# Optimization experiments

Hardware: AMD Instinct MI355X
Metric: run time of the kernel (lower is better)

Reference implementation:

```python
import jax, jax.numpy as jnp
import numpy as np

B, M, T, D, V = 16, 4096, 4, 256, 40000
HOPS, NLAYER, CONV_MAX = 3, 3, 512
PAD = 1  # PAD_token: embedding row zeroed (padding_idx)


def setup_inputs() -> dict:
    key = jax.random.key(0)
    ks = jax.random.split(key, 10)
    story = jax.random.randint(ks[0], (B, M, T), 0, V)
    conv_len = jax.random.randint(ks[1], (B,), 1, CONV_MAX)
    kb_len = jax.random.randint(ks[2], (B,), 0, M - CONV_MAX)
    query = jax.random.normal(ks[3], (B, 1, D), jnp.float32)
    history_outputs = jax.random.normal(ks[4], (B, CONV_MAX, D), jnp.float32)
    query_vector = jax.random.normal(ks[5], (B, D), jnp.float32)
    global_pointer = jax.random.uniform(ks[6], (B, M), jnp.float32)
    # hop+1 embedding tables, N(0, 0.1), padding row zeroed
    C_emb = jax.random.normal(ks[7], (HOPS + 1, V, D), jnp.float32) * 0.1
    C_emb = C_emb.at[:, PAD, :].set(0.0)
    Tg_w = jax.random.normal(ks[8], (HOPS + 1, D, D), jnp.float32) * 0.05
    Tg_b = jnp.zeros((HOPS + 1, D), jnp.float32)
    FW_w = jax.random.normal(ks[9], (D, D), jnp.float32) * 0.05
    FW_b = jnp.zeros((D,), jnp.float32)
    return dict(story=story, kb_len=kb_len, conv_len=conv_len, query=query,
                history_outputs=history_outputs, query_vector=query_vector,
                global_pointer=global_pointer, C_emb=C_emb, Tg_w=Tg_w,
                Tg_b=Tg_b, FW_w=FW_w, FW_b=FW_b)


def _add_lm(mem, kb_len, conv_len, hist):
    # mem: [B,M,D]; add hist[b, 0:conv_len[b]] into mem[b, kb_len[b]:kb_len[b]+conv_len[b]]
    j = jnp.arange(mem.shape[1])[None, :]                       # [1,M]
    start = kb_len[:, None]
    mask = (j >= start) & (j < start + conv_len[:, None])       # [B,M]
    idx = jnp.clip(j - start, 0, hist.shape[1] - 1)             # [B,M]
    gathered = jnp.take_along_axis(hist, idx[..., None], axis=1)  # [B,M,D]
    return mem + jnp.where(mask[..., None], gathered, 0.0)


def _embed(table, story, kb_len, conv_len, hist):
    # bag-of-words over the mem-token axis, then LM-embedding add
    e = jnp.sum(table[story], axis=2)                           # [B,M,D]
    return _add_lm(e, kb_len, conv_len, hist)


def reference(story, kb_len, conv_len, query, history_outputs, query_vector,
              global_pointer, C_emb, Tg_w, Tg_b, FW_w, FW_b):
    # ---- load_memory (eval mode: dropout is identity; ablationH/G = False) ----
    q = query[:, 0, :]                                          # [B,D]
    last_u = None
    m_story = None
    for layer in range(NLAYER):
        iq = q
        if layer > 0:
            g = jax.nn.sigmoid(iq @ Tg_w[0].T + Tg_b[0])
            iq = last_u[0] * g + iq * (1.0 - g)
        u = [iq]
        m_story = []
        embC = None
        for hop in range(HOPS):
            embA = _embed(C_emb[hop], story, kb_len, conv_len, history_outputs)
            logit = jnp.einsum('bmd,bd->bm', embA, u[-1])
            prob = jax.nn.softmax(logit, axis=1)
            embC = _embed(C_emb[hop + 1], story, kb_len, conv_len, history_outputs)
            o_k = jnp.einsum('bm,bmd->bd', prob, embC)
            u_k = u[-1] + o_k
            if layer > 0:
                g = jax.nn.sigmoid(u_k @ Tg_w[hop + 1].T + Tg_b[hop + 1])
                u_k = last_u[hop + 1] * g + u_k * (1.0 - g)
            u.append(u_k)
            m_story.append(embA)
        m_story.append(embC)
        last_u = u
        q = jax.nn.relu(u[-1] @ FW_w.T + FW_b)
    # ---- forward (decoder-side read over last layer's memories) ----
    uf = query_vector
    psoft = None
    logits = None
    for hop in range(HOPS):
        mA = m_story[hop] * global_pointer[:, :, None]
        logits = jnp.einsum('bmd,bd->bm', mA, uf)
        psoft = jax.nn.softmax(logits, axis=1)
        mC = m_story[hop + 1] * global_pointer[:, :, None]
        uf = uf + jnp.einsum('bm,bmd->bd', psoft, mC)
    return (psoft, logits, uf, m_story[-1])
```

## Files before the change

kernel.cpp:

```cpp
#include <hip/hip_runtime.h>
#include <math.h>

#define Bdim 16
#define Mdim 4096
#define Tdim 4
#define Ddim 256
#define Vdim 40000
#define CONVMAX 512
#define MT 64

__global__ void init_kernel(const float* __restrict__ qv, float* __restrict__ uf) {
    int b = blockIdx.x, i = threadIdx.x;
    uf[(size_t)b * Ddim + i] = qv[(size_t)b * Ddim + i];
}

__global__ void qk_kernel(const int* __restrict__ story, const int* __restrict__ kb_len,
                          const int* __restrict__ conv_len, const float* __restrict__ hist,
                          const float* __restrict__ tab, const float* __restrict__ uf,
                          const float* __restrict__ gp, float* __restrict__ logits) {
    int tid = threadIdx.x, wave = tid >> 6, lane = tid & 63;
    int row0 = blockIdx.x * 16 + wave * 4;
    int b = row0 >> 12;
    int d4 = lane * 4;
    const float4 uv = *(const float4*)(uf + (size_t)b * Ddim + d4);
    int kb = kb_len[b], cl = conv_len[b];
#pragma unroll
    for (int r = 0; r < 4; ++r) {
        int row = row0 + r;
        int m = row & (Mdim - 1);
        const int* st = story + (size_t)row * Tdim;
        float4 acc = make_float4(0.f, 0.f, 0.f, 0.f);
#pragma unroll
        for (int t = 0; t < Tdim; ++t) {
            const float4 v = *(const float4*)(tab + (size_t)st[t] * Ddim + d4);
            acc.x += v.x; acc.y += v.y; acc.z += v.z; acc.w += v.w;
        }
        if (m >= kb && m < kb + cl) {
            const float4 h = *(const float4*)(hist + ((size_t)b * CONVMAX + (m - kb)) * Ddim + d4);
            acc.x += h.x; acc.y += h.y; acc.z += h.z; acc.w += h.w;
        }
        float p = acc.x * uv.x + acc.y * uv.y + acc.z * uv.z + acc.w * uv.w;
#pragma unroll
        for (int off = 32; off > 0; off >>= 1) p += __shfl_xor(p, off, 64);
        if (lane == 0) logits[row] = p * gp[row];
    }
}

__global__ void stats_kernel(const float* __restrict__ logits, float* __restrict__ maxv,
                             float* __restrict__ rsum) {
    int b = blockIdx.x, tid = threadIdx.x;
    __shared__ float sh[256];
    const float* lg = logits + (size_t)b * Mdim;
    float mx = -INFINITY;
    for (int i = tid; i < Mdim; i += 256) mx = fmaxf(mx, lg[i]);
    sh[tid] = mx; __syncthreads();
    for (int s = 128; s > 0; s >>= 1) { if (tid < s) sh[tid] = fmaxf(sh[tid], sh[tid + s]); __syncthreads(); }
    float bm = sh[0]; __syncthreads();
    float sm = 0.f;
    for (int i = tid; i < Mdim; i += 256) sm += expf(lg[i] - bm);
    sh[tid] = sm; __syncthreads();
    for (int s = 128; s > 0; s >>= 1) { if (tid < s) sh[tid] += sh[tid + s]; __syncthreads(); }
    if (tid == 0) { maxv[b] = bm; rsum[b] = 1.0f / sh[0]; }
}

__global__ void att_kernel(const int* __restrict__ story, const int* __restrict__ kb_len,
                           const int* __restrict__ conv_len, const float* __restrict__ hist,
                           const float* __restrict__ tab, const float* __restrict__ logits,
                           const float* __restrict__ maxv, const float* __restrict__ rsum,
                           const float* __restrict__ gp,
                           float* __restrict__ uf_acc, float* __restrict__ out_m,
                           float* __restrict__ out_psoft) {
    int bid = blockIdx.x;
    int b  = bid / (Mdim / MT);
    int m0 = (bid % (Mdim / MT)) * MT;
    int tid = threadIdx.x, wave = tid >> 6, lane = tid & 63;
    int d4 = lane * 4;
    __shared__ float prob[MT];
    __shared__ float4 red[4][64];
    if (tid < MT) {
        size_t row = (size_t)b * Mdim + m0 + tid;
        float pn = expf(logits[row] - maxv[b]) * rsum[b];
        if (out_psoft) out_psoft[row] = pn;
        prob[tid] = pn * gp[row];
    }
    __syncthreads();
    int kb = kb_len[b], cl = conv_len[b];
    float4 acc = make_float4(0.f, 0.f, 0.f, 0.f);
#pragma unroll 4
    for (int mm = wave; mm < MT; mm += 4) {
        int m = m0 + mm;
        size_t row = (size_t)b * Mdim + m;
        const int* st = story + row * Tdim;
        float4 v = make_float4(0.f, 0.f, 0.f, 0.f);
#pragma unroll
        for (int t = 0; t < Tdim; ++t) {
            const float4 w = *(const float4*)(tab + (size_t)st[t] * Ddim + d4);
            v.x += w.x; v.y += w.y; v.z += w.z; v.w += w.w;
        }
        if (m >= kb && m < kb + cl) {
            const float4 h = *(const float4*)(hist + ((size_t)b * CONVMAX + (m - kb)) * Ddim + d4);
            v.x += h.x; v.y += h.y; v.z += h.z; v.w += h.w;
        }
        if (out_m) *(float4*)(out_m + row * Ddim + d4) = v;
        float p = prob[mm];
        acc.x += p * v.x; acc.y += p * v.y; acc.z += p * v.z; acc.w += p * v.w;
    }
    red[wave][lane] = acc;
    __syncthreads();
    if (wave == 0) {
        float4 a0 = red[0][lane], a1 = red[1][lane], a2 = red[2][lane], a3 = red[3][lane];
        float* dst = uf_acc + (size_t)b * Ddim + d4;
        atomicAdd(dst + 0, a0.x + a1.x + a2.x + a3.x);
        atomicAdd(dst + 1, a0.y + a1.y + a2.y + a3.y);
        atomicAdd(dst + 2, a0.z + a1.z + a2.z + a3.z);
        atomicAdd(dst + 3, a0.w + a1.w + a2.w + a3.w);
    }
}

extern "C" void kernel_launch(void* const* d_in, const int* in_sizes, int n_in,
                              void* d_out, int out_size, void* d_ws, size_t ws_size,
                              hipStream_t stream) {
    const int*   story        = (const int*)d_in[0];
    const int*   kb_len       = (const int*)d_in[1];
    const int*   conv_len     = (const int*)d_in[2];
    const float* hist         = (const float*)d_in[4];
    const float* query_vector = (const float*)d_in[5];
    const float* gp           = (const float*)d_in[6];
    const float* C_emb        = (const float*)d_in[7];

    float* out        = (float*)d_out;
    float* out_psoft  = out;
    float* out_logits = out + (size_t)Bdim * Mdim;
    float* out_uf     = out + 2 * (size_t)Bdim * Mdim;
    float* out_m      = out + 2 * (size_t)Bdim * Mdim + (size_t)Bdim * Ddim;

    float* ws = (float*)d_ws;
    float* logits = ws;
    float* maxv   = logits + (size_t)Bdim * Mdim;
    float* rsum   = maxv + Bdim;

    const size_t TAB = (size_t)Vdim * Ddim;
    const float* tab0 = C_emb;
    const float* tab1 = C_emb + TAB;
    const float* tab2 = C_emb + 2 * TAB;
    const float* tab3 = C_emb + 3 * TAB;

    const int QK_GRID  = Bdim * Mdim / 16;
    const int ATT_GRID = Bdim * (Mdim / MT);

    init_kernel<<<Bdim, Ddim, 0, stream>>>(query_vector, out_uf);

    qk_kernel<<<QK_GRID, 256, 0, stream>>>(story, kb_len, conv_len, hist,
                                           tab0, query_vector, gp, logits);
    stats_kernel<<<Bdim, 256, 0, stream>>>(logits, maxv, rsum);
    att_kernel<<<ATT_GRID, 256, 0, stream>>>(story, kb_len, conv_len, hist,
                                             tab1, logits, maxv, rsum, gp,
                                             out_uf, nullptr, nullptr);
    qk_kernel<<<QK_GRID, 256, 0, stream>>>(story, kb_len, conv_len, hist,
                                           tab1, out_uf, gp, logits);
    stats_kernel<<<Bdim, 256, 0, stream>>>(logits, maxv, rsum);
    att_kernel<<<ATT_GRID, 256, 0, stream>>>(story, kb_len, conv_len, hist,
                                             tab2, logits, maxv, rsum, gp,
                                             out_uf, nullptr, nullptr);
    qk_kernel<<<QK_GRID, 256, 0, stream>>>(story, kb_len, conv_len, hist,
                                           tab2, out_uf, gp, out_logits);
    stats_kernel<<<Bdim, 256, 0, stream>>>(out_logits, maxv, rsum);
    att_kernel<<<ATT_GRID, 256, 0, stream>>>(story, kb_len, conv_len, hist,
                                             tab3, out_logits, maxv, rsum, gp,
                                             out_uf, out_m, out_psoft);
}
```

Measured before the change: 490.4 us.

## Fuse all hops into one cooperative kernel using vocabulary-space dot products

Replaces the per-hop gather kernels with a single cooperative persistent kernel that uses grid-wide syncs between stages. Logits are computed by first taking the product of the whole embedding table with the query (a V×B dot matrix) and then summing the entries for each story's tokens. For hops 0 and 1 the weighted sum is scattered into vocabulary weights and reduced against the table, so no per-row gather is needed. Only the final hop materializes out_m, using nontemporal stores. This streams the full 40k-row table for every hop instead of gathering 4 rows per memory slot, and adds many grid syncs, heavy atomics on the weight buffer, and occupancy limits from the cooperative launch.

```diff
diff --git a/kernel.cpp b/kernel.cpp
--- a/kernel.cpp
+++ b/kernel.cpp
@@ -1,5 +1,8 @@
 #include <hip/hip_runtime.h>
+#include <hip/hip_cooperative_groups.h>
 #include <math.h>
+
+namespace cg = cooperative_groups;
 
 #define Bdim 16
 #define Mdim 4096
@@ -7,113 +10,310 @@
 #define Ddim 256
 #define Vdim 40000
 #define CONVMAX 512
+
+#define NT 256
+
+#define DOT_VT 64
+#define DOT_TILES (Vdim / DOT_VT)
+#define DOT_KC 64
+#define HD_JPB 32
+#define HD_TILES (Bdim * (CONVMAX / HD_JPB))
+#define WS_VT 50
+#define WS_TILES (Vdim / WS_VT)
+#define WH_JPB 64
+#define WH_TILES (Bdim * (CONVMAX / WH_JPB))
 #define MT 64
-
-__global__ void init_kernel(const float* __restrict__ qv, float* __restrict__ uf) {
-    int b = blockIdx.x, i = threadIdx.x;
-    uf[(size_t)b * Ddim + i] = qv[(size_t)b * Ddim + i];
+#define ATT_TILES (Bdim * (Mdim / MT))
+
+typedef float f32x4 __attribute__((ext_vector_type(4)));
+static __device__ inline void nt_store4(float* p, float4 v) {
+    f32x4 x = {v.x, v.y, v.z, v.w};
+    __builtin_nontemporal_store(x, (f32x4*)p);
 }
-
-__global__ void qk_kernel(const int* __restrict__ story, const int* __restrict__ kb_len,
-                          const int* __restrict__ conv_len, const float* __restrict__ hist,
-                          const float* __restrict__ tab, const float* __restrict__ uf,
-                          const float* __restrict__ gp, float* __restrict__ logits) {
-    int tid = threadIdx.x, wave = tid >> 6, lane = tid & 63;
-    int row0 = blockIdx.x * 16 + wave * 4;
-    int b = row0 >> 12;
-    int d4 = lane * 4;
-    const float4 uv = *(const float4*)(uf + (size_t)b * Ddim + d4);
-    int kb = kb_len[b], cl = conv_len[b];
-#pragma unroll
-    for (int r = 0; r < 4; ++r) {
-        int row = row0 + r;
-        int m = row & (Mdim - 1);
-        const int* st = story + (size_t)row * Tdim;
-        float4 acc = make_float4(0.f, 0.f, 0.f, 0.f);
-#pragma unroll
-        for (int t = 0; t < Tdim; ++t) {
-            const float4 v = *(const float4*)(tab + (size_t)st[t] * Ddim + d4);
-            acc.x += v.x; acc.y += v.y; acc.z += v.z; acc.w += v.w;
+static __device__ inline void nt_store1(float* p, float v) {
+    __builtin_nontemporal_store(v, p);
+}
+
+__global__ __launch_bounds__(NT, 4) void fused_kernel(
+    const int* __restrict__ story, const int* __restrict__ kb_len,
+    const int* __restrict__ conv_len, const float* __restrict__ hist,
+    const float* __restrict__ qv, const float* __restrict__ gp,
+    const float* __restrict__ C_emb,
+    float* __restrict__ out_psoft, float* __restrict__ out_logits,
+    float* __restrict__ uf, float* __restrict__ out_m,
+    float* __restrict__ D, float* __restrict__ w,
+    float* __restrict__ Hdot, float* __restrict__ pwin,
+    float* __restrict__ logits, float* __restrict__ blockmax,
+    float* __restrict__ blocksum, float* __restrict__ partial,
+    float* __restrict__ histpart, float* __restrict__ attpart)
+{
+    cg::grid_group grid = cg::this_grid();
+    const int nb = gridDim.x;
+    const int tid = threadIdx.x;
+    const int wave = tid >> 6, lane = tid & 63;
+    const int d4 = lane * 4;
+    __shared__ __align__(16) float smem[80 * (DOT_KC + 4)];
+
+    const size_t TAB = (size_t)Vdim * Ddim;
+
+    for (int h = 0; h < 3; ++h) {
+        const float* qt = C_emb + (size_t)h * TAB;
+        const float* vt = C_emb + (size_t)(h + 1) * TAB;
+        const float* ufsrc = (h == 0) ? qv : uf;
+        float* lgbuf = (h == 2) ? out_logits : logits;
+
+        for (int it = blockIdx.x; it < DOT_TILES + HD_TILES; it += nb) {
+            if (it < DOT_TILES) {
+                float (*tl)[DOT_KC + 4]  = (float (*)[DOT_KC + 4])smem;
+                float (*ufl)[DOT_KC + 4] = (float (*)[DOT_KC + 4])(smem + DOT_VT * (DOT_KC + 4));
+                const int v0 = it * DOT_VT;
+                const int vA = (tid >> 3) * 2, vB = vA + 1;
+                const int bA = (tid & 7) * 2,  bB = bA + 1;
+                float aA0 = 0.f, aA1 = 0.f, aB0 = 0.f, aB1 = 0.f;
+                for (int kc = 0; kc < Ddim; kc += DOT_KC) {
+                    __syncthreads();
+#pragma unroll
+                    for (int i = 0; i < 4; ++i) {
+                        int idx = tid + i * NT;
+                        int r = idx >> 4, c4 = idx & 15;
+                        *(float4*)(&tl[r][c4 * 4]) =
+                            *(const float4*)(qt + (size_t)(v0 + r) * Ddim + kc + c4 * 4);
+                    }
+                    {
+                        int r = tid >> 4, c4 = tid & 15;
+                        *(float4*)(&ufl[r][c4 * 4]) =
+                            *(const float4*)(ufsrc + (size_t)r * Ddim + kc + c4 * 4);
+                    }
+                    __syncthreads();
+#pragma unroll
+                    for (int k4 = 0; k4 < DOT_KC / 4; ++k4) {
+                        const float4 a  = *(const float4*)(&tl[vA][k4 * 4]);
+                        const float4 c  = *(const float4*)(&tl[vB][k4 * 4]);
+                        const float4 u0 = *(const float4*)(&ufl[bA][k4 * 4]);
+                        const float4 u1 = *(const float4*)(&ufl[bB][k4 * 4]);
+                        aA0 += a.x*u0.x + a.y*u0.y + a.z*u0.z + a.w*u0.w;
+                        aA1 += a.x*u1.x + a.y*u1.y + a.z*u1.z + a.w*u1.w;
+                        aB0 += c.x*u0.x + c.y*u0.y + c.z*u0.z + c.w*u0.w;
+                        aB1 += c.x*u1.x + c.y*u1.y + c.z*u1.z + c.w*u1.w;
+                    }
+                }
+                size_t base = (size_t)(v0 + vA) * Bdim;
+                D[base + bA] = aA0;  D[base + bB] = aA1;
+                D[base + Bdim + bA] = aB0;  D[base + Bdim + bB] = aB1;
+            } else {
+                int r = it - DOT_TILES;
+                int b = r >> 4, j0 = (r & 15) * HD_JPB;
+                const float4 u = *(const float4*)(ufsrc + (size_t)b * Ddim + d4);
+                for (int j = j0 + wave; j < j0 + HD_JPB; j += 4) {
+                    const float4 hv = *(const float4*)(hist + ((size_t)b * CONVMAX + j) * Ddim + d4);
+                    float s = hv.x*u.x + hv.y*u.y + hv.z*u.z + hv.w*u.w;
+#pragma unroll
+                    for (int off = 32; off > 0; off >>= 1) s += __shfl_xor(s, off, 64);
+                    if (lane == 0) Hdot[b * CONVMAX + j] = s;
+                }
+            }
         }
-        if (m >= kb && m < kb + cl) {
-            const float4 h = *(const float4*)(hist + ((size_t)b * CONVMAX + (m - kb)) * Ddim + d4);
-            acc.x += h.x; acc.y += h.y; acc.z += h.z; acc.w += h.w;
+        grid.sync();
+
+        {
+            const int nzero = (h < 2) ? (Vdim * Bdim / 1024 + Bdim * CONVMAX / 1024) : 0;
+            for (int it = blockIdx.x; it < 256 + nzero; it += nb) {
+                if (it < 256) {
+                    int row = it * NT + tid;
+                    int b = row >> 12, m = row & (Mdim - 1);
+                    const int4 st = *(const int4*)(story + (size_t)row * Tdim);
+                    float l = D[st.x*Bdim + b] + D[st.y*Bdim + b] + D[st.z*Bdim + b] + D[st.w*Bdim + b];
+                    unsigned j = (unsigned)(m - kb_len[b]);
+                    if (j < (unsigned)conv_len[b]) l += Hdot[b * CONVMAX + j];
+                    l *= gp[row];
+                    lgbuf[row] = l;
+                    float* sh = smem;
+                    __syncthreads();
+                    sh[tid] = l; __syncthreads();
+                    for (int s = 128; s > 0; s >>= 1) { if (tid < s) sh[tid] = fmaxf(sh[tid], sh[tid + s]); __syncthreads(); }
+                    float bm = sh[0]; __syncthreads();
+                    sh[tid] = expf(l - bm); __syncthreads();
+                    for (int s = 128; s > 0; s >>= 1) { if (tid < s) sh[tid] += sh[tid + s]; __syncthreads(); }
+                    if (tid == 0) { blockmax[it] = bm; blocksum[it] = sh[0]; }
+                } else if (it < 256 + Vdim * Bdim / 1024) {
+                    int r = it - 256;
+                    *(float4*)(w + (size_t)r * 1024 + tid * 4) = make_float4(0.f, 0.f, 0.f, 0.f);
+                } else {
+                    int r = it - (256 + Vdim * Bdim / 1024);
+                    *(float4*)(pwin + (size_t)r * 1024 + tid * 4) = make_float4(0.f, 0.f, 0.f, 0.f);
+                }
+            }
         }
-        float p = acc.x * uv.x + acc.y * uv.y + acc.z * uv.z + acc.w * uv.w;
-#pragma unroll
-        for (int off = 32; off > 0; off >>= 1) p += __shfl_xor(p, off, 64);
-        if (lane == 0) logits[row] = p * gp[row];
-    }
-}
-
-__global__ void stats_kernel(const float* __restrict__ logits, float* __restrict__ maxv,
-                             float* __restrict__ rsum) {
-    int b = blockIdx.x, tid = threadIdx.x;
-    __shared__ float sh[256];
-    const float* lg = logits + (size_t)b * Mdim;
-    float mx = -INFINITY;
-    for (int i = tid; i < Mdim; i += 256) mx = fmaxf(mx, lg[i]);
-    sh[tid] = mx; __syncthreads();
-    for (int s = 128; s > 0; s >>= 1) { if (tid < s) sh[tid] = fmaxf(sh[tid], sh[tid + s]); __syncthreads(); }
-    float bm = sh[0]; __syncthreads();
-    float sm = 0.f;
-    for (int i = tid; i < Mdim; i += 256) sm += expf(lg[i] - bm);
-    sh[tid] = sm; __syncthreads();
-    for (int s = 128; s > 0; s >>= 1) { if (tid < s) sh[tid] += sh[tid + s]; __syncthreads(); }
-    if (tid == 0) { maxv[b] = bm; rsum[b] = 1.0f / sh[0]; }
-}
-
-__global__ void att_kernel(const int* __restrict__ story, const int* __restrict__ kb_len,
-                           const int* __restrict__ conv_len, const float* __restrict__ hist,
-                           const float* __restrict__ tab, const float* __restrict__ logits,
-                           const float* __restrict__ maxv, const float* __restrict__ rsum,
-                           const float* __restrict__ gp,
-                           float* __restrict__ uf_acc, float* __restrict__ out_m,
-                           float* __restrict__ out_psoft) {
-    int bid = blockIdx.x;
-    int b  = bid / (Mdim / MT);
-    int m0 = (bid % (Mdim / MT)) * MT;
-    int tid = threadIdx.x, wave = tid >> 6, lane = tid & 63;
-    int d4 = lane * 4;
-    __shared__ float prob[MT];
-    __shared__ float4 red[4][64];
-    if (tid < MT) {
-        size_t row = (size_t)b * Mdim + m0 + tid;
-        float pn = expf(logits[row] - maxv[b]) * rsum[b];
-        if (out_psoft) out_psoft[row] = pn;
-        prob[tid] = pn * gp[row];
-    }
-    __syncthreads();
-    int kb = kb_len[b], cl = conv_len[b];
-    float4 acc = make_float4(0.f, 0.f, 0.f, 0.f);
-#pragma unroll 4
-    for (int mm = wave; mm < MT; mm += 4) {
-        int m = m0 + mm;
-        size_t row = (size_t)b * Mdim + m;
-        const int* st = story + row * Tdim;
-        float4 v = make_float4(0.f, 0.f, 0.f, 0.f);
-#pragma unroll
-        for (int t = 0; t < Tdim; ++t) {
-            const float4 w = *(const float4*)(tab + (size_t)st[t] * Ddim + d4);
-            v.x += w.x; v.y += w.y; v.z += w.z; v.w += w.w;
+        grid.sync();
+
+        if (h < 2) {
+            for (int it = blockIdx.x; it < 256; it += nb) {
+                int b = it >> 4;
+                float M = -INFINITY;
+#pragma unroll
+                for (int jj = 0; jj < 16; ++jj) M = fmaxf(M, blockmax[b * 16 + jj]);
+                float S = 0.f;
+#pragma unroll
+                for (int jj = 0; jj < 16; ++jj) S += blocksum[b * 16 + jj] * expf(blockmax[b * 16 + jj] - M);
+                float rs = 1.0f / S;
+                int row = it * NT + tid;
+                int m = row & (Mdim - 1);
+                float p = expf(logits[row] - M) * rs * gp[row];
+                const int4 st = *(const int4*)(story + (size_t)row * Tdim);
+                atomicAdd(&w[st.x * Bdim + b], p);
+                atomicAdd(&w[st.y * Bdim + b], p);
+                atomicAdd(&w[st.z * Bdim + b], p);
+                atomicAdd(&w[st.w * Bdim + b], p);
+                unsigned j = (unsigned)(m - kb_len[b]);
+                if (j < (unsigned)conv_len[b]) pwin[b * CONVMAX + j] = p;
+            }
+            grid.sync();
+
+            for (int it = blockIdx.x; it < WS_TILES + WH_TILES; it += nb) {
+                if (it < WS_TILES) {
+                    float* wsl = smem;
+                    int v0 = it * WS_VT;
+                    __syncthreads();
+                    for (int i = tid; i < WS_VT * Bdim; i += NT) wsl[i] = w[(size_t)v0 * Bdim + i];
+                    __syncthreads();
+                    int b0 = wave * 4;
+                    float4 a0 = make_float4(0.f,0.f,0.f,0.f), a1 = a0, a2 = a0, a3 = a0;
+                    for (int v = 0; v < WS_VT; ++v) {
+                        const float4 t = *(const float4*)(vt + (size_t)(v0 + v) * Ddim + d4);
+                        float w0 = wsl[v * Bdim + b0],     w1 = wsl[v * Bdim + b0 + 1];
+                        float w2 = wsl[v * Bdim + b0 + 2], w3 = wsl[v * Bdim + b0 + 3];
+                        a0.x += w0*t.x; a0.y += w0*t.y; a0.z += w0*t.z; a0.w += w0*t.w;
+                        a1.x += w1*t.x; a1.y += w1*t.y; a1.z += w1*t.z; a1.w += w1*t.w;
+                        a2.x += w2*t.x; a2.y += w2*t.y; a2.z += w2*t.z; a2.w += w2*t.w;
+                        a3.x += w3*t.x; a3.y += w3*t.y; a3.z += w3*t.z; a3.w += w3*t.w;
+                    }
+                    *(float4*)(&partial[((size_t)(b0 + 0) * WS_TILES + it) * Ddim + d4]) = a0;
+                    *(float4*)(&partial[((size_t)(b0 + 1) * WS_TILES + it) * Ddim + d4]) = a1;
+                    *(float4*)(&partial[((size_t)(b0 + 2) * WS_TILES + it) * Ddim + d4]) = a2;
+                    *(float4*)(&partial[((size_t)(b0 + 3) * WS_TILES + it) * Ddim + d4]) = a3;
+                } else {
+                    int r = it - WS_TILES;
+                    int b = r >> 3, j0 = (r & 7) * WH_JPB;
+                    float* sp = smem;
+                    __syncthreads();
+                    if (tid < WH_JPB) sp[tid] = pwin[b * CONVMAX + j0 + tid];
+                    __syncthreads();
+                    float acc = 0.f;
+                    const float* hb = hist + ((size_t)b * CONVMAX + j0) * Ddim + tid;
+#pragma unroll 8
+                    for (int j = 0; j < WH_JPB; ++j) acc += sp[j] * hb[(size_t)j * Ddim];
+                    histpart[((size_t)b * 8 + (r & 7)) * Ddim + tid] = acc;
+                }
+            }
+            grid.sync();
+
+            for (int it = blockIdx.x; it < Bdim; it += nb) {
+                int b = it;
+                float4 acc = make_float4(0.f, 0.f, 0.f, 0.f);
+                for (int s = wave; s < WS_TILES; s += 4) {
+                    const float4 p4 = *(const float4*)(&partial[((size_t)b * WS_TILES + s) * Ddim + d4]);
+                    acc.x += p4.x; acc.y += p4.y; acc.z += p4.z; acc.w += p4.w;
+                }
+                if (wave == 0) {
+#pragma unroll
+                    for (int c = 0; c < 8; ++c) {
+                        const float4 hp = *(const float4*)(&histpart[((size_t)b * 8 + c) * Ddim + d4]);
+                        acc.x += hp.x; acc.y += hp.y; acc.z += hp.z; acc.w += hp.w;
+                    }
+                }
+                float4* red = (float4*)smem;
+                __syncthreads();
+                red[wave * 64 + lane] = acc;
+                __syncthreads();
+                if (wave == 0) {
+                    float4 r0 = red[lane], r1 = red[64 + lane], r2 = red[128 + lane], r3 = red[192 + lane];
+                    const float* basep = (h == 0) ? qv : uf;
+                    float4 bv = *(const float4*)(basep + (size_t)b * Ddim + d4);
+                    bv.x += r0.x + r1.x + r2.x + r3.x;
+                    bv.y += r0.y + r1.y + r2.y + r3.y;
+                    bv.z += r0.z + r1.z + r2.z + r3.z;
+                    bv.w += r0.w + r1.w + r2.w + r3.w;
+                    *(float4*)(uf + (size_t)b * Ddim + d4) = bv;
+                }
+            }
+            grid.sync();
+        } else {
+            for (int it = blockIdx.x; it < ATT_TILES; it += nb) {
+                int b = it >> 6, m0 = (it & 63) * MT;
+                float* prob = smem;
+                float4* red = (float4*)(smem + 64);
+                __syncthreads();
+                if (tid < MT) {
+                    float M = -INFINITY;
+#pragma unroll
+                    for (int jj = 0; jj < 16; ++jj) M = fmaxf(M, blockmax[b * 16 + jj]);
+                    float S = 0.f;
+#pragma unroll
+                    for (int jj = 0; jj < 16; ++jj) S += blocksum[b * 16 + jj] * expf(blockmax[b * 16 + jj] - M);
+                    float rs = 1.0f / S;
+                    size_t row = (size_t)b * Mdim + m0 + tid;
+                    float pn = expf(out_logits[row] - M) * rs;
+                    nt_store1(out_psoft + row, pn);
+                    prob[tid] = pn * gp[row];
+                }
+                __syncthreads();
+                int kb = kb_len[b], cl = conv_len[b];
+                float4 acc = make_float4(0.f, 0.f, 0.f, 0.f);
+                for (int mm = wave; mm < MT; mm += 4) {
+                    int m = m0 + mm;
+                    size_t row = (size_t)b * Mdim + m;
+                    const int* st = story + row * Tdim;
+                    float4 v = make_float4(0.f, 0.f, 0.f, 0.f);
+#pragma unroll
+                    for (int t = 0; t < Tdim; ++t) {
+                        const float4 tv = *(const float4*)(vt + (size_t)st[t] * Ddim + d4);
+                        v.x += tv.x; v.y += tv.y; v.z += tv.z; v.w += tv.w;
+                    }
+                    if (m >= kb && m < kb + cl) {
+                        const float4 hv = *(const float4*)(hist + ((size_t)b * CONVMAX + (m - kb)) * Ddim + d4);
+                        v.x += hv.x; v.y += hv.y; v.z += hv.z; v.w += hv.w;
+                    }
+                    nt_store4(out_m + row * Ddim + d4, v);
+                    float p = prob[mm];
+                    acc.x += p * v.x; acc.y += p * v.y; acc.z += p * v.z; acc.w += p * v.w;
+                }
+                red[wave * 64 + lane] = acc;
+                __syncthreads();
+                if (wave == 0) {
+                    float4 a0 = red[lane], a1 = red[64 + lane], a2 = red[128 + lane], a3 = red[192 + lane];
+                    float4 t4;
+                    t4.x = a0.x + a1.x + a2.x + a3.x;
+                    t4.y = a0.y + a1.y + a2.y + a3.y;
+                    t4.z = a0.z + a1.z + a2.z + a3.z;
+                    t4.w = a0.w + a1.w + a2.w + a3.w;
+                    *(float4*)(&attpart[((size_t)b * 64 + (it & 63)) * Ddim + d4]) = t4;
+                }
+            }
+            grid.sync();
+
+            for (int it = blockIdx.x; it < Bdim; it += nb) {
+                int b = it;
+                float4 acc = make_float4(0.f, 0.f, 0.f, 0.f);
+                for (int c = wave; c < 64; c += 4) {
+                    const float4 p4 = *(const float4*)(&attpart[((size_t)b * 64 + c) * Ddim + d4]);
+                    acc.x += p4.x; acc.y += p4.y; acc.z += p4.z; acc.w += p4.w;
+                }
+                float4* red = (float4*)smem;
+                __syncthreads();
+                red[wave * 64 + lane] = acc;
+                __syncthreads();
+                if (wave == 0) {
+                    float4 r0 = red[lane], r1 = red[64 + lane], r2 = red[128 + lane], r3 = red[192 + lane];
+                    float* dst = uf + (size_t)b * Ddim + d4;
+                    float4 cur = *(const float4*)dst;
+                    cur.x += r0.x + r1.x + r2.x + r3.x;
+                    cur.y += r0.y + r1.y + r2.y + r3.y;
+                    cur.z += r0.z + r1.z + r2.z + r3.z;
+                    cur.w += r0.w + r1.w + r2.w + r3.w;
+                    *(float4*)dst = cur;
+                }
+            }
         }
-        if (m >= kb && m < kb + cl) {
-            const float4 h = *(const float4*)(hist + ((size_t)b * CONVMAX + (m - kb)) * Ddim + d4);
-            v.x += h.x; v.y += h.y; v.z += h.z; v.w += h.w;
-        }
-        if (out_m) *(float4*)(out_m + row * Ddim + d4) = v;
-        float p = prob[mm];
-        acc.x += p * v.x; acc.y += p * v.y; acc.z += p * v.z; acc.w += p * v.w;
-    }
-    red[wave][lane] = acc;
-    __syncthreads();
-    if (wave == 0) {
-        float4 a0 = red[0][lane], a1 = red[1][lane], a2 = red[2][lane], a3 = red[3][lane];
-        float* dst = uf_acc + (size_t)b * Ddim + d4;
-        atomicAdd(dst + 0, a0.x + a1.x + a2.x + a3.x);
-        atomicAdd(dst + 1, a0.y + a1.y + a2.y + a3.y);
-        atomicAdd(dst + 2, a0.z + a1.z + a2.z + a3.z);
-        atomicAdd(dst + 3, a0.w + a1.w + a2.w + a3.w);
     }
 }
 
@@ -134,38 +334,39 @@
     float* out_uf     = out + 2 * (size_t)Bdim * Mdim;
     float* out_m      = out + 2 * (size_t)Bdim * Mdim + (size_t)Bdim * Ddim;
 
-    float* ws = (float*)d_ws;
-    float* logits = ws;
-    float* maxv   = logits + (size_t)Bdim * Mdim;
-    float* rsum   = maxv + Bdim;
-
-    const size_t TAB = (size_t)Vdim * Ddim;
-    const float* tab0 = C_emb;
-    const float* tab1 = C_emb + TAB;
-    const float* tab2 = C_emb + 2 * TAB;
-    const float* tab3 = C_emb + 3 * TAB;
-
-    const int QK_GRID  = Bdim * Mdim / 16;
-    const int ATT_GRID = Bdim * (Mdim / MT);
-
-    init_kernel<<<Bdim, Ddim, 0, stream>>>(query_vector, out_uf);
-
-    qk_kernel<<<QK_GRID, 256, 0, stream>>>(story, kb_len, conv_len, hist,
-                                           tab0, query_vector, gp, logits);
-    stats_kernel<<<Bdim, 256, 0, stream>>>(logits, maxv, rsum);
-    att_kernel<<<ATT_GRID, 256, 0, stream>>>(story, kb_len, conv_len, hist,
-                                             tab1, logits, maxv, rsum, gp,
-                                             out_uf, nullptr, nullptr);
-    qk_kernel<<<QK_GRID, 256, 0, stream>>>(story, kb_len, conv_len, hist,
-                                           tab1, out_uf, gp, logits);
-    stats_kernel<<<Bdim, 256, 0, stream>>>(logits, maxv, rsum);
-    att_kernel<<<ATT_GRID, 256, 0, stream>>>(story, kb_len, conv_len, hist,
-                                             tab2, logits, maxv, rsum, gp,
-                                             out_uf, nullptr, nullptr);
-    qk_kernel<<<QK_GRID, 256, 0, stream>>>(story, kb_len, conv_len, hist,
-                                           tab2, out_uf, gp, out_logits);
-    stats_kernel<<<Bdim, 256, 0, stream>>>(out_logits, maxv, rsum);
-    att_kernel<<<ATT_GRID, 256, 0, stream>>>(story, kb_len, conv_len, hist,
-                                             tab3, out_logits, maxv, rsum, gp,
-                                             out_uf, out_m, out_psoft);
+    float* wsp = (float*)d_ws;
+    float* D        = wsp;
+    float* w        = D + (size_t)Vdim * Bdim;
+    float* Hdot     = w + (size_t)Vdim * Bdim;
+    float* pwin     = Hdot + (size_t)Bdim * CONVMAX;
+    float* logits   = pwin + (size_t)Bdim * CONVMAX;
+    float* blockmax = logits + (size_t)Bdim * Mdim;
+    float* blocksum = blockmax + 256;
+    float* partial  = blocksum + 256;
+    float* histpart = partial + (size_t)Bdim * WS_TILES * Ddim;
+    float* attpart  = histpart + (size_t)Bdim * 8 * Ddim;
+
+    static int coopGrid = 0;
+    if (coopGrid == 0) {
+        int nblk = 0;
+        hipOccupancyMaxActiveBlocksPerMultiprocessor(&nblk, fused_kernel, NT, 0);
+        if (nblk < 1) nblk = 1;
+        hipDeviceProp_t prop;
+        int dev = 0;
+        hipGetDevice(&dev);
+        hipGetDeviceProperties(&prop, dev);
+        long cap = (long)nblk * prop.multiProcessorCount;
+        coopGrid = (int)((cap < 1024) ? cap : 1024);
+    }
+
+    void* args[] = {
+        (void*)&story, (void*)&kb_len, (void*)&conv_len, (void*)&hist,
+        (void*)&query_vector, (void*)&gp, (void*)&C_emb,
+        (void*)&out_psoft, (void*)&out_logits, (void*)&out_uf, (void*)&out_m,
+        (void*)&D, (void*)&w, (void*)&Hdot, (void*)&pwin, (void*)&logits,
+        (void*)&blockmax, (void*)&blocksum, (void*)&partial, (void*)&histpart,
+        (void*)&attpart
+    };
+    hipLaunchCooperativeKernel((void*)fused_kernel, dim3(coopGrid), dim3(NT),
+                               args, 0, stream);
 }
```

Result: slower. 1.417 ms (+188.9%).
